# Kernel tuning notes

Measured on AMD Instinct MI355X. Metric: run time of the kernel, lower is better.

Reference implementation:

```python
import jax, jax.numpy as jnp
import numpy as np

N_FFT = 2048
HOP = 512


def setup_inputs() -> dict:
    key = jax.random.key(0)
    x = jax.random.normal(key, (16, 1048576), dtype=jnp.float32)
    return {"x": x}


def reference(x):
    # causal buffer: fresh module state -> zeros of shape [..., frames_out*hop]
    frames_out = N_FFT // HOP - 1  # 3
    buf = jnp.zeros(x.shape[:-1] + (frames_out * HOP,), dtype=x.dtype)
    xc = jnp.concatenate([buf, x], axis=-1)  # [B, T + 1536]
    L = xc.shape[-1]
    num_frames = (L - N_FFT) // HOP + 1
    # strided framing via gather: out[..., f, t] = xc[..., f*hop + t]
    idx = jnp.arange(num_frames)[:, None] * HOP + jnp.arange(N_FFT)[None, :]
    return xc[..., idx]  # [B, num_frames, n_fft]
```

## Files before the change

kernel.cpp:

```cpp
#include <hip/hip_runtime.h>
#include <hip/hip_bf16.h>


#define T4_PER_B   262144u
#define R4         128u
#define QI_COUNT   2051u
#define NFRAMES    2048u

__global__ __launch_bounds__(256) void scatter_frames(
    const float4* __restrict__ x4, float4* __restrict__ out4)
{
    unsigned int gid = blockIdx.x * blockDim.x + threadIdx.x;
    const unsigned int total = 16u * QI_COUNT * R4;
    if (gid >= total) return;

    unsigned int r4 = gid & (R4 - 1u);
    unsigned int rest = gid >> 7;
    unsigned int qi = rest % QI_COUNT;
    unsigned int b  = rest / QI_COUNT;
    int q = (int)qi - 3;

    float4 v;
    if (q >= 0) {
        v = x4[(size_t)b * T4_PER_B + (unsigned)q * R4 + r4];
    } else {
        v = make_float4(0.f, 0.f, 0.f, 0.f);
    }

    size_t obase = ((size_t)b * NFRAMES) * 512u + r4;
#pragma unroll
    for (int k = 0; k < 4; ++k) {
        int f = q + k;
        if (f >= 0 && f < (int)NFRAMES) {
            out4[obase + (size_t)f * 512u + (unsigned)(3 - k) * 128u] = v;
        }
    }
}

extern "C" void kernel_launch(void* const* d_in, const int* in_sizes, int n_in,
                              void* d_out, int out_size, void* d_ws, size_t ws_size,
                              hipStream_t stream) {
    const float4* x4 = (const float4*)d_in[0];
    float4* out4 = (float4*)d_out;
    const unsigned int total = 16u * QI_COUNT * R4;
    dim3 block(256);
    dim3 grid((total + 255u) / 256u);
    scatter_frames<<<grid, block, 0, stream>>>(x4, out4);
}
```

Measured before the change: 66.05 us.

## Batch four segments per thread with 2D grid and nontemporal loads/stores

Each thread now handles four 512-float segments instead of one. The batch index moves to grid.y, which removes the per-thread division and modulo, and the index arithmetic drops from 64-bit to 32-bit. Loads and stores use nontemporal builtins so the write-heavy stream (each input chunk is written four times) bypasses cache retention. The intent is more memory operations in flight per thread with fewer launched threads. The risks are fewer waves to hide latency and 32-bit offsets that must stay in range for the 128M-element output.

```diff
diff --git a/kernel.cpp b/kernel.cpp
--- a/kernel.cpp
+++ b/kernel.cpp
@@ -2,37 +2,52 @@
 #include <hip/hip_bf16.h>
 
 
+typedef float f4 __attribute__((ext_vector_type(4)));
+
 #define T4_PER_B   262144u
 #define R4         128u
-#define QI_COUNT   2051u
-#define NFRAMES    2048u
+#define QI_COUNT   2051
+#define NFRAMES    2048
+#define F4_PER_FRAME 512u
 
 __global__ __launch_bounds__(256) void scatter_frames(
-    const float4* __restrict__ x4, float4* __restrict__ out4)
+    const f4* __restrict__ x4, f4* __restrict__ out4)
 {
-    unsigned int gid = blockIdx.x * blockDim.x + threadIdx.x;
-    const unsigned int total = 16u * QI_COUNT * R4;
-    if (gid >= total) return;
+    const unsigned tid  = threadIdx.x;
+    const unsigned r4   = tid & (R4 - 1u);
+    const unsigned sub  = tid >> 7;
+    const unsigned b    = blockIdx.y;
+    const unsigned qi0  = blockIdx.x * 8u + sub;
 
-    unsigned int r4 = gid & (R4 - 1u);
-    unsigned int rest = gid >> 7;
-    unsigned int qi = rest % QI_COUNT;
-    unsigned int b  = rest / QI_COUNT;
-    int q = (int)qi - 3;
+    const f4 zero = (f4){0.f, 0.f, 0.f, 0.f};
+    const unsigned xbase = b * T4_PER_B + r4;
+    const unsigned obase = b * (NFRAMES * F4_PER_FRAME) + r4;
 
-    float4 v;
-    if (q >= 0) {
-        v = x4[(size_t)b * T4_PER_B + (unsigned)q * R4 + r4];
-    } else {
-        v = make_float4(0.f, 0.f, 0.f, 0.f);
+    f4 v[4];
+    int q[4];
+#pragma unroll
+    for (int j = 0; j < 4; ++j) {
+        unsigned qi = qi0 + 2u * (unsigned)j;
+        q[j] = (int)qi - 3;
+        if (qi < (unsigned)QI_COUNT && q[j] >= 0) {
+            v[j] = __builtin_nontemporal_load(&x4[xbase + (unsigned)q[j] * R4]);
+        } else {
+            v[j] = zero;
+        }
     }
 
-    size_t obase = ((size_t)b * NFRAMES) * 512u + r4;
 #pragma unroll
-    for (int k = 0; k < 4; ++k) {
-        int f = q + k;
-        if (f >= 0 && f < (int)NFRAMES) {
-            out4[obase + (size_t)f * 512u + (unsigned)(3 - k) * 128u] = v;
+    for (int j = 0; j < 4; ++j) {
+        unsigned qi = qi0 + 2u * (unsigned)j;
+        if (qi >= (unsigned)QI_COUNT) continue;
+#pragma unroll
+        for (int k = 0; k < 4; ++k) {
+            int f = q[j] + k;
+            if (f >= 0 && f < NFRAMES) {
+                __builtin_nontemporal_store(
+                    v[j], &out4[obase + (unsigned)f * F4_PER_FRAME
+                                + (unsigned)(3 - k) * R4]);
+            }
         }
     }
 }
@@ -40,10 +55,9 @@
 extern "C" void kernel_launch(void* const* d_in, const int* in_sizes, int n_in,
                               void* d_out, int out_size, void* d_ws, size_t ws_size,
                               hipStream_t stream) {
-    const float4* x4 = (const float4*)d_in[0];
-    float4* out4 = (float4*)d_out;
-    const unsigned int total = 16u * QI_COUNT * R4;
+    const f4* x4 = (const f4*)d_in[0];
+    f4* out4 = (f4*)d_out;
     dim3 block(256);
-    dim3 grid((total + 255u) / 256u);
+    dim3 grid(257, 16);
     scatter_frames<<<grid, block, 0, stream>>>(x4, out4);
 }
```

After: 71.87 us. 1.09x slower.
